# Optimization experiments

Hardware: AMD Instinct MI355X
Metric: run time of the kernel (lower is better)

The kernel has to match this reference:

```python
import jax, jax.numpy as jnp
import numpy as np

B, L, ENC, DEC, ATT = 256, 196, 2048, 512, 512

def setup_inputs() -> dict:
    key = jax.random.key(0)
    ks = jax.random.split(key, 8)
    s_enc = 1.0 / np.sqrt(ENC); s_dec = 1.0 / np.sqrt(DEC); s_att = 1.0 / np.sqrt(ATT)
    return {
        "encoder_out": jax.random.normal(ks[0], (B, L, ENC), dtype=jnp.float32),
        "decoder_hidden": jax.random.normal(ks[1], (B, DEC), dtype=jnp.float32),
        "W_enc": jax.random.uniform(ks[2], (ENC, ATT), jnp.float32, -s_enc, s_enc),
        "b_enc": jax.random.uniform(ks[3], (ATT,), jnp.float32, -s_enc, s_enc),
        "W_dec": jax.random.uniform(ks[4], (DEC, ATT), jnp.float32, -s_dec, s_dec),
        "b_dec": jax.random.uniform(ks[5], (ATT,), jnp.float32, -s_dec, s_dec),
        "W_att": jax.random.uniform(ks[6], (ATT, 1), jnp.float32, -s_att, s_att),
        "b_att": jax.random.uniform(ks[7], (1,), jnp.float32, -s_att, s_att),
    }

def reference(encoder_out, decoder_hidden, W_enc, b_enc, W_dec, b_dec, W_att, b_att):
    # encoder_att: [B, L, A]; decoder_att: [B, A]
    encoder_att = jnp.einsum('ble,ea->bla', encoder_out, W_enc) + b_enc
    decoder_att = decoder_hidden @ W_dec + b_dec
    hidden = jax.nn.relu(encoder_att + decoder_att[:, None, :])  # [B, L, A]
    att = jnp.einsum('bla,a->bl', hidden, W_att[:, 0]) + b_att[0]  # [B, L]
    alpha = jax.nn.softmax(att, axis=1)  # softmax over sequence dim
    awe = jnp.einsum('ble,bl->be', encoder_out, alpha)  # weighted sum
    return awe, alpha
```

## Files before the change

### kernel.cpp

```cpp
#include <hip/hip_runtime.h>
#include <hip/hip_bf16.h>
#include <stdint.h>

#define NB 256
#define NL 196
#define NE 2048
#define ND 512
#define NA 512
#define NM (NB * NL)

typedef __attribute__((ext_vector_type(4))) float f32x4;
typedef __attribute__((ext_vector_type(8))) short bf16x8;

static __device__ __forceinline__ unsigned short f2bf(float f) {
  __hip_bfloat16 h = __float2bfloat16(f);
  unsigned short u;
  __builtin_memcpy(&u, &h, 2);
  return u;
}

__global__ __launch_bounds__(512) void k_prep(
    const float* __restrict__ W, unsigned short* __restrict__ Bp,
    const float* __restrict__ dec, const float* __restrict__ Wd,
    const float* __restrict__ bd, const float* __restrict__ be,
    float* __restrict__ d2) {
  if (blockIdx.x < 256) {
    int t = blockIdx.x * 512 + threadIdx.x;
    int lane = t & 63;
    int kt32 = (t >> 6) & 63;
    int ntile = t >> 12;
    int col = ntile * 16 + (lane & 15);
    int k0 = kt32 * 32 + ((lane >> 4) << 3);
    bf16x8 o;
#pragma unroll
    for (int j = 0; j < 8; ++j) o[j] = (short)f2bf(W[(size_t)(k0 + j) * NA + col]);
    *reinterpret_cast<bf16x8*>(Bp + ((size_t)t << 3)) = o;
  } else {
    __shared__ float dh[ND];
    int b = blockIdx.x - 256, tid = threadIdx.x;
    dh[tid] = dec[(size_t)b * ND + tid];
    __syncthreads();
    float s = bd[tid] + be[tid];
#pragma unroll 8
    for (int e = 0; e < ND; ++e) s = fmaf(dh[e], Wd[(size_t)e * NA + tid], s);
    d2[(size_t)b * NA + tid] = s;
  }
}

#define BM 64
#define BK 64
#define KT (NE / BK)

__global__ __launch_bounds__(512, 4) void k_main(
    const float* __restrict__ A,
    const unsigned short* __restrict__ Bp,
    const float* __restrict__ d2,
    const float* __restrict__ Watt,
    const float* __restrict__ batt,
    float* __restrict__ att)
{
  __shared__ unsigned short As[2][BM * BK];
  __shared__ float att_w[8][BM];

  const int tid = threadIdx.x;
  const int lane = tid & 63;
  const int wid = tid >> 6;
  const int lq = lane >> 4;
  const int lr = lane & 15;
  const int row0 = blockIdx.x * BM;

  f32x4 acc[4][4];
#pragma unroll
  for (int mf = 0; mf < 4; ++mf)
#pragma unroll
    for (int r = 0; r < 4; ++r) {
      int rowg = row0 + mf * 16 + lq * 4 + r;
      int bb = rowg / NL;
      const float* d2r = d2 + (size_t)bb * NA + wid * 64 + lr;
#pragma unroll
      for (int nf = 0; nf < 4; ++nf) acc[mf][nf][r] = d2r[nf * 16];
    }

  const int srow = tid >> 3;
  const int skc = tid & 7;
  const float* ag = A + (size_t)(row0 + srow) * NE + skc * 8;
  const int swz_w = srow * 64 + ((skc ^ (srow & 7)) << 3);

  auto cvt_store = [&](int buf, const f32x4& a, const f32x4& b) {
    bf16x8 o;
    o[0] = (short)f2bf(a[0]); o[1] = (short)f2bf(a[1]);
    o[2] = (short)f2bf(a[2]); o[3] = (short)f2bf(a[3]);
    o[4] = (short)f2bf(b[0]); o[5] = (short)f2bf(b[1]);
    o[6] = (short)f2bf(b[2]); o[7] = (short)f2bf(b[3]);
    *reinterpret_cast<bf16x8*>(&As[buf][swz_w]) = o;
  };

  {
    f32x4 p0 = *reinterpret_cast<const f32x4*>(ag);
    f32x4 p1 = *reinterpret_cast<const f32x4*>(ag + 4);
    cvt_store(0, p0, p1);
  }
  __syncthreads();

  const unsigned short* bpw = Bp + (size_t)(wid * 4) * 32768 + lane * 8;

  for (int kt = 0; kt < KT; ++kt) {
    const int cur = kt & 1;
    f32x4 n0, n1;
    if (kt < KT - 1) {
      const float* agn = ag + (size_t)(kt + 1) * BK;
      n0 = *reinterpret_cast<const f32x4*>(agn);
      n1 = *reinterpret_cast<const f32x4*>(agn + 4);
    }
    bf16x8 bf[4][2];
#pragma unroll
    for (int nf = 0; nf < 4; ++nf)
#pragma unroll
      for (int ks = 0; ks < 2; ++ks)
        bf[nf][ks] = *reinterpret_cast<const bf16x8*>(bpw + (size_t)nf * 32768 + (kt * 2 + ks) * 512);
#pragma unroll
    for (int ks = 0; ks < 2; ++ks)
#pragma unroll
      for (int mf = 0; mf < 4; ++mf) {
        const int rrow = mf * 16 + lr;
        const int chunk = (ks * 4 + lq) ^ (lr & 7);
        bf16x8 af = *reinterpret_cast<const bf16x8*>(&As[cur][rrow * 64 + (chunk << 3)]);
#pragma unroll
        for (int nf = 0; nf < 4; ++nf)
          acc[mf][nf] = __builtin_amdgcn_mfma_f32_16x16x32_bf16(af, bf[nf][ks], acc[mf][nf], 0, 0, 0);
      }
    if (kt < KT - 1) cvt_store(cur ^ 1, n0, n1);
    __syncthreads();
  }

  float w[4];
#pragma unroll
  for (int nf = 0; nf < 4; ++nf) w[nf] = Watt[wid * 64 + nf * 16 + lr];
#pragma unroll
  for (int mf = 0; mf < 4; ++mf)
#pragma unroll
    for (int r = 0; r < 4; ++r) {
      float s = 0.f;
#pragma unroll
      for (int nf = 0; nf < 4; ++nf) s = fmaf(fmaxf(acc[mf][nf][r], 0.f), w[nf], s);
      s += __shfl_xor(s, 1);
      s += __shfl_xor(s, 2);
      s += __shfl_xor(s, 4);
      s += __shfl_xor(s, 8);
      if (lr == 0) att_w[wid][mf * 16 + lq * 4 + r] = s;
    }
  __syncthreads();
  if (tid < BM) {
    float s = 0.f;
#pragma unroll
    for (int wv = 0; wv < 8; ++wv) s += att_w[wv][tid];
    att[row0 + tid] = s + batt[0];
  }
}

__global__ __launch_bounds__(512) void k_awe(
    const float* __restrict__ enc, const float* __restrict__ att,
    float* __restrict__ alpha_out, float* __restrict__ awe) {
  __shared__ float al[256];
  const int b = blockIdx.x, tid = threadIdx.x;

  if (tid < 64) {
    const int lane = tid;
    const float* ar = att + (size_t)b * NL;
    float v[4];
#pragma unroll
    for (int i = 0; i < 4; ++i) {
      int l = i * 64 + lane;
      v[i] = (l < NL) ? ar[l] : -1e30f;
    }
    float m = fmaxf(fmaxf(v[0], v[1]), fmaxf(v[2], v[3]));
#pragma unroll
    for (int o = 32; o >= 1; o >>= 1) m = fmaxf(m, __shfl_xor(m, o));
    float e[4];
    float s = 0.f;
#pragma unroll
    for (int i = 0; i < 4; ++i) {
      int l = i * 64 + lane;
      e[i] = (l < NL) ? __expf(v[i] - m) : 0.f;
      s += e[i];
    }
#pragma unroll
    for (int o = 32; o >= 1; o >>= 1) s += __shfl_xor(s, o);
    float inv = 1.f / s;
#pragma unroll
    for (int i = 0; i < 4; ++i) {
      int l = i * 64 + lane;
      if (l < NL) {
        float a = e[i] * inv;
        al[l] = a;
        alpha_out[(size_t)b * NL + l] = a;
      }
    }
  }
  __syncthreads();

  const float* ep = enc + (size_t)b * NL * NE + tid * 4;
  f32x4 a0 = {0.f, 0.f, 0.f, 0.f}, a1 = a0, a2 = a0, a3 = a0;
#pragma unroll 2
  for (int l = 0; l < NL; l += 4) {
    f32x4 v0 = *reinterpret_cast<const f32x4*>(ep + (size_t)l * NE);
    f32x4 v1 = *reinterpret_cast<const f32x4*>(ep + (size_t)(l + 1) * NE);
    f32x4 v2 = *reinterpret_cast<const f32x4*>(ep + (size_t)(l + 2) * NE);
    f32x4 v3 = *reinterpret_cast<const f32x4*>(ep + (size_t)(l + 3) * NE);
    float c0 = al[l], c1 = al[l + 1], c2 = al[l + 2], c3 = al[l + 3];
#pragma unroll
    for (int j = 0; j < 4; ++j) {
      a0[j] = fmaf(c0, v0[j], a0[j]);
      a1[j] = fmaf(c1, v1[j], a1[j]);
      a2[j] = fmaf(c2, v2[j], a2[j]);
      a3[j] = fmaf(c3, v3[j], a3[j]);
    }
  }
  f32x4 s4;
#pragma unroll
  for (int j = 0; j < 4; ++j) s4[j] = (a0[j] + a1[j]) + (a2[j] + a3[j]);
  *reinterpret_cast<f32x4*>(awe + (size_t)b * NE + tid * 4) = s4;
}

extern "C" void kernel_launch(void* const* d_in, const int* in_sizes, int n_in,
                              void* d_out, int out_size, void* d_ws, size_t ws_size,
                              hipStream_t stream) {
  const float* enc  = (const float*)d_in[0];
  const float* dec  = (const float*)d_in[1];
  const float* Wenc = (const float*)d_in[2];
  const float* benc = (const float*)d_in[3];
  const float* Wdec = (const float*)d_in[4];
  const float* bdec = (const float*)d_in[5];
  const float* Watt = (const float*)d_in[6];
  const float* batt = (const float*)d_in[7];

  float* awe   = (float*)d_out;
  float* alpha = (float*)d_out + (size_t)NB * NE;

  char* ws = (char*)d_ws;
  unsigned short* Bp = (unsigned short*)ws;
  float* d2  = (float*)(ws + (size_t)2 * 1024 * 1024);
  float* att = (float*)(ws + (size_t)2 * 1024 * 1024 + 512 * 1024);

  k_prep<<<dim3(512), dim3(512), 0, stream>>>(Wenc, Bp, dec, Wdec, bdec, benc, d2);
  k_main<<<dim3(NM / BM), dim3(512), 0, stream>>>(enc, Bp, d2, Watt, batt, att);
  k_awe<<<dim3(NB), dim3(512), 0, stream>>>(enc, att, alpha, awe);
}
```

Before: 256.8 us.

## Deepen A prefetch, batch decoder GEMV, split awe blocks, raise MFMA priority

The main GEMM now prefetches the fp32 encoder tile two k-steps ahead instead of one, and raises wave priority around the MFMA block with s_setprio. Its launch bound drops from 4 to 2 waves-per-EU hint, giving more registers for the deeper prefetch at the cost of occupancy. The decoder projection now processes 8 batch rows per block so each Wd load is reused 8 times, cutting prep blocks from 512 to 288. The awe kernel is split into two 256-thread blocks per batch row, each covering half the feature dimension, for more parallelism at the cost of computing the softmax twice.

New measurement: 350.5 us. 36.5% more time.

```diff
diff --git a/kernel.cpp b/kernel.cpp
--- a/kernel.cpp
+++ b/kernel.cpp
@@ -36,14 +36,23 @@
     for (int j = 0; j < 8; ++j) o[j] = (short)f2bf(W[(size_t)(k0 + j) * NA + col]);
     *reinterpret_cast<bf16x8*>(Bp + ((size_t)t << 3)) = o;
   } else {
-    __shared__ float dh[ND];
-    int b = blockIdx.x - 256, tid = threadIdx.x;
-    dh[tid] = dec[(size_t)b * ND + tid];
+    __shared__ float dh[8][ND];
+    const int b0 = (blockIdx.x - 256) * 8, tid = threadIdx.x;
+#pragma unroll
+    for (int j = 0; j < 8; ++j) dh[j][tid] = dec[(size_t)(b0 + j) * ND + tid];
     __syncthreads();
-    float s = bd[tid] + be[tid];
-#pragma unroll 8
-    for (int e = 0; e < ND; ++e) s = fmaf(dh[e], Wd[(size_t)e * NA + tid], s);
-    d2[(size_t)b * NA + tid] = s;
+    float base = bd[tid] + be[tid];
+    float acc[8];
+#pragma unroll
+    for (int j = 0; j < 8; ++j) acc[j] = base;
+#pragma unroll 4
+    for (int e = 0; e < ND; ++e) {
+      float w = Wd[(size_t)e * NA + tid];
+#pragma unroll
+      for (int j = 0; j < 8; ++j) acc[j] = fmaf(dh[j][e], w, acc[j]);
+    }
+#pragma unroll
+    for (int j = 0; j < 8; ++j) d2[(size_t)(b0 + j) * NA + tid] = acc[j];
   }
 }
 
@@ -51,7 +60,7 @@
 #define BK 64
 #define KT (NE / BK)
 
-__global__ __launch_bounds__(512, 4) void k_main(
+__global__ __launch_bounds__(512, 2) void k_main(
     const float* __restrict__ A,
     const unsigned short* __restrict__ Bp,
     const float* __restrict__ d2,
@@ -95,10 +104,13 @@
     *reinterpret_cast<bf16x8*>(&As[buf][swz_w]) = o;
   };
 
+  f32x4 h0, h1;
   {
-    f32x4 p0 = *reinterpret_cast<const f32x4*>(ag);
-    f32x4 p1 = *reinterpret_cast<const f32x4*>(ag + 4);
-    cvt_store(0, p0, p1);
+    f32x4 c0 = *reinterpret_cast<const f32x4*>(ag);
+    f32x4 c1 = *reinterpret_cast<const f32x4*>(ag + 4);
+    h0 = *reinterpret_cast<const f32x4*>(ag + BK);
+    h1 = *reinterpret_cast<const f32x4*>(ag + BK + 4);
+    cvt_store(0, c0, c1);
   }
   __syncthreads();
 
@@ -106,11 +118,11 @@
 
   for (int kt = 0; kt < KT; ++kt) {
     const int cur = kt & 1;
-    f32x4 n0, n1;
-    if (kt < KT - 1) {
-      const float* agn = ag + (size_t)(kt + 1) * BK;
-      n0 = *reinterpret_cast<const f32x4*>(agn);
-      n1 = *reinterpret_cast<const f32x4*>(agn + 4);
+    f32x4 m0, m1;
+    if (kt + 2 < KT) {
+      const float* agn = ag + (size_t)(kt + 2) * BK;
+      m0 = *reinterpret_cast<const f32x4*>(agn);
+      m1 = *reinterpret_cast<const f32x4*>(agn + 4);
     }
     bf16x8 bf[4][2];
 #pragma unroll
@@ -118,6 +130,7 @@
 #pragma unroll
       for (int ks = 0; ks < 2; ++ks)
         bf[nf][ks] = *reinterpret_cast<const bf16x8*>(bpw + (size_t)nf * 32768 + (kt * 2 + ks) * 512);
+    __builtin_amdgcn_s_setprio(1);
 #pragma unroll
     for (int ks = 0; ks < 2; ++ks)
 #pragma unroll
@@ -129,7 +142,9 @@
         for (int nf = 0; nf < 4; ++nf)
           acc[mf][nf] = __builtin_amdgcn_mfma_f32_16x16x32_bf16(af, bf[nf][ks], acc[mf][nf], 0, 0, 0);
       }
-    if (kt < KT - 1) cvt_store(cur ^ 1, n0, n1);
+    __builtin_amdgcn_s_setprio(0);
+    if (kt < KT - 1) cvt_store(cur ^ 1, h0, h1);
+    if (kt + 2 < KT) { h0 = m0; h1 = m1; }
     __syncthreads();
   }
 
@@ -158,11 +173,11 @@
   }
 }
 
-__global__ __launch_bounds__(512) void k_awe(
+__global__ __launch_bounds__(256) void k_awe(
     const float* __restrict__ enc, const float* __restrict__ att,
     float* __restrict__ alpha_out, float* __restrict__ awe) {
   __shared__ float al[256];
-  const int b = blockIdx.x, tid = threadIdx.x;
+  const int b = blockIdx.x >> 1, ch = blockIdx.x & 1, tid = threadIdx.x;
 
   if (tid < 64) {
     const int lane = tid;
@@ -193,13 +208,13 @@
       if (l < NL) {
         float a = e[i] * inv;
         al[l] = a;
-        alpha_out[(size_t)b * NL + l] = a;
+        if (ch == 0) alpha_out[(size_t)b * NL + l] = a;
       }
     }
   }
   __syncthreads();
 
-  const float* ep = enc + (size_t)b * NL * NE + tid * 4;
+  const float* ep = enc + (size_t)b * NL * NE + ch * 1024 + tid * 4;
   f32x4 a0 = {0.f, 0.f, 0.f, 0.f}, a1 = a0, a2 = a0, a3 = a0;
 #pragma unroll 2
   for (int l = 0; l < NL; l += 4) {
@@ -219,7 +234,7 @@
   f32x4 s4;
 #pragma unroll
   for (int j = 0; j < 4; ++j) s4[j] = (a0[j] + a1[j]) + (a2[j] + a3[j]);
-  *reinterpret_cast<f32x4*>(awe + (size_t)b * NE + tid * 4) = s4;
+  *reinterpret_cast<f32x4*>(awe + (size_t)b * NE + ch * 1024 + tid * 4) = s4;
 }
 
 extern "C" void kernel_launch(void* const* d_in, const int* in_sizes, int n_in,
@@ -242,7 +257,7 @@
   float* d2  = (float*)(ws + (size_t)2 * 1024 * 1024);
   float* att = (float*)(ws + (size_t)2 * 1024 * 1024 + 512 * 1024);
 
-  k_prep<<<dim3(512), dim3(512), 0, stream>>>(Wenc, Bp, dec, Wdec, bdec, benc, d2);
+  k_prep<<<dim3(288), dim3(512), 0, stream>>>(Wenc, Bp, dec, Wdec, bdec, benc, d2);
   k_main<<<dim3(NM / BM), dim3(512), 0, stream>>>(enc, Bp, d2, Watt, batt, att);
-  k_awe<<<dim3(NB), dim3(512), 0, stream>>>(enc, att, alpha, awe);
-}
+  k_awe<<<dim3(NB * 2), dim3(256), 0, stream>>>(enc, att, alpha, awe);
+}
```
